# Optimization experiments

Hardware: AMD Instinct MI355X
Metric: run time of the kernel (lower is better)

The kernel has to match this reference:

```python
import math
import jax, jax.numpy as jnp
import numpy as np

B, N, D = 4, 4096, 1024
H = 16
DK = D // H  # 64
M = 256      # nb_features
EPS = 1e-6


def _gorf(key, n_rows, n_cols):
    """Gaussian orthogonal random matrix (n_rows, n_cols), stacked orthonormal
    blocks with chi-distributed row lengths (Performer GORF)."""
    blocks, rows_left = [], n_rows
    while rows_left > 0:
        br = min(n_cols, rows_left)
        key, k1, k2 = jax.random.split(key, 3)
        u = jax.random.normal(k1, (n_cols, n_cols), dtype=jnp.float32)
        q, r = jnp.linalg.qr(u)
        q = q * jnp.sign(jnp.diagonal(r))[None, :]  # q @ diag(sign(diag(r)))
        g = jax.random.normal(k2, (br, n_cols), dtype=jnp.float32)
        lengths = jnp.linalg.norm(g, axis=1, keepdims=True)
        blocks.append(q[:br] * lengths)
        rows_left -= br
    return jnp.concatenate(blocks, axis=0)


def setup_inputs() -> dict:
    key = jax.random.key(0)
    ks = jax.random.split(key, 8)
    x = jax.random.normal(ks[0], (B, N, D), dtype=jnp.float32)
    # True = PAD
    key_padding_mask = jax.random.randint(ks[1], (B, N), 0, 2).astype(jnp.bool_)
    # Linear params (xavier-scale init; exact scheme irrelevant to the math)
    Wqkv = jax.random.normal(ks[2], (3 * D, D), dtype=jnp.float32) * 0.02
    bqkv = jnp.zeros((3 * D,), dtype=jnp.float32)
    Wout = jax.random.normal(ks[3], (D, D), dtype=jnp.float32) * 0.02
    bout = jnp.zeros((D,), dtype=jnp.float32)
    # Per-head GORF omega, scaled by sqrt(dk) as in _draw_features
    omega = jnp.stack(
        [_gorf(jax.random.fold_in(ks[4], h), M, DK) for h in range(H)], axis=0
    ) * math.sqrt(DK)  # (H, M, dk)
    return {"x": x, "key_padding_mask": key_padding_mask, "Wqkv": Wqkv,
            "bqkv": bqkv, "Wout": Wout, "bout": bout, "omega": omega}


def _phi_exp(t, omega):
    # t: (B,H,N,dk) -> (B,H,N,M)
    proj = jnp.einsum('bhnd,hmd->bhnm', t, omega)
    sq_norm = 0.5 * jnp.sum(t * t, axis=-1, keepdims=True)
    z = proj - sq_norm
    z = z - jnp.max(z, axis=-1, keepdims=True)          # stabilize
    return jnp.exp(z) / math.sqrt(M + 1e-6)


def reference(x, key_padding_mask, Wqkv, bqkv, Wout, bout, omega):
    qkv = x @ Wqkv.T + bqkv                              # (B,N,3D)
    Q, K, V = jnp.split(qkv, 3, axis=-1)
    split = lambda t: t.reshape(B, N, H, DK).transpose(0, 2, 1, 3)  # (B,H,N,dk)
    Q, K, V = split(Q), split(K), split(V)
    valid_bool = ~key_padding_mask                       # (B,N), True=real token
    valid = valid_bool[:, None, :, None].astype(x.dtype) # (B,1,N,1)
    Qp = _phi_exp(Q, omega)                              # (B,H,N,M)
    Kp = _phi_exp(K, omega) * valid                      # zero PAD keys
    KV = jnp.einsum('bhnm,bhnd->bhmd', Kp, V)            # (B,H,M,dk)
    ksum = jnp.sum(Kp, axis=2)                           # (B,H,M)
    num = jnp.einsum('bhnm,bhmd->bhnd', Qp, KV)          # (B,H,N,dk)
    den = jnp.einsum('bhnm,bhm->bhn', Qp, ksum)[..., None] + EPS
    ctx = num / den                                      # (B,H,N,dk)
    out = ctx.transpose(0, 2, 1, 3).reshape(B, N, D)     # merge heads
    out = out @ Wout.T + bout
    out = out * valid_bool[..., None].astype(out.dtype)  # PAD queries -> exact 0
    return out
```

## Files before the change

kernel.cpp:

```cpp
#include <hip/hip_runtime.h>
#include <hip/hip_bf16.h>
#include <math.h>

#define B_  4
#define N_  4096
#define D_  1024
#define H_  16
#define DK_ 64
#define M_  256
#define R_  (B_*N_)
#define EPS_ 1e-6f
#define VTROWS_ 80
#define KVROWS_ 128
#define PHK_PAD 68
#define PHQ_PAD 264

typedef __bf16 bf16;
typedef __bf16 bf16x4 __attribute__((ext_vector_type(4)));
typedef __bf16 bf16x8 __attribute__((ext_vector_type(8)));
typedef _Float16 f16;
typedef _Float16 f16x4 __attribute__((ext_vector_type(4)));
typedef _Float16 f16x8 __attribute__((ext_vector_type(8)));
typedef float  f32x4  __attribute__((ext_vector_type(4)));

#define GLD(gp, lp) __builtin_amdgcn_global_load_lds( \
    (const __attribute__((address_space(1))) void*)(gp), \
    (__attribute__((address_space(3))) void*)(lp), 16, 0, 0)

#define BAR_()   __builtin_amdgcn_s_barrier()
#define SBAR_()  __builtin_amdgcn_sched_barrier(0)
#define PRIO1_() __builtin_amdgcn_s_setprio(1)
#define PRIO0_() __builtin_amdgcn_s_setprio(0)
#define LGK0_()  do { asm volatile("s_waitcnt lgkmcnt(0)"); SBAR_(); } while (0)
#define LGK8_()  asm volatile("s_waitcnt lgkmcnt(8)")
#define VMC4_()  do { asm volatile("s_waitcnt vmcnt(4)"); SBAR_(); } while (0)

__global__ __launch_bounds__(256)
void prep_all(const float* __restrict__ x, f16* __restrict__ xh,
              const float* __restrict__ Wqkv, f16* __restrict__ Wh,
              const float* __restrict__ omega, f16* __restrict__ omhi,
              f16* __restrict__ omlo,
              const float* __restrict__ Wout, bf16* __restrict__ Wob,
              float* __restrict__ KVt32, bf16* __restrict__ VT)
{
    const int bid = blockIdx.x, tid = threadIdx.x;
    if (bid < 16384) {
        int i = bid*256 + tid;
        float4 v = ((const float4*)x)[i];
        f16x4 h = { (f16)v.x, (f16)v.y, (f16)v.z, (f16)v.w };
        ((f16x4*)xh)[i] = h;
    } else if (bid < 19456) {
        int i = (bid - 16384)*256 + tid;
        float4 v = ((const float4*)Wqkv)[i];
        f16x4 h = { (f16)v.x, (f16)v.y, (f16)v.z, (f16)v.w };
        ((f16x4*)Wh)[i] = h;
    } else if (bid < 19712) {
        int i = (bid - 19456)*256 + tid;
        float4 v = ((const float4*)omega)[i];
        f16x4 h = { (f16)v.x, (f16)v.y, (f16)v.z, (f16)v.w };
        ((f16x4*)omhi)[i] = h;
        f16x4 l = { (f16)(v.x - (float)h[0]), (f16)(v.y - (float)h[1]),
                    (f16)(v.z - (float)h[2]), (f16)(v.w - (float)h[3]) };
        ((f16x4*)omlo)[i] = l;
    } else if (bid < 20736) {
        int i = (bid - 19712)*256 + tid;
        float4 v = ((const float4*)Wout)[i];
        bf16x4 h = { (bf16)v.x, (bf16)v.y, (bf16)v.z, (bf16)v.w };
        ((bf16x4*)Wob)[i] = h;
    } else if (bid < 22016) {
        int i = (bid - 20736)*256 + tid;
        ((float4*)KVt32)[i] = make_float4(0.f, 0.f, 0.f, 0.f);
    } else {
        int i = (bid - 22016)*256 + tid;
        int bh  = i >> 13;
        int rem = i & 8191;
        int row = 64 + (rem >> 9);
        int n8  = rem & 511;
        bf16 val = (row == 64) ? (bf16)1.0f : (bf16)0.0f;
        bf16x8 pk = { val, val, val, val, val, val, val, val };
        *(bf16x8*)&VT[((size_t)bh*VTROWS_ + row)*N_ + n8*8] = pk;
    }
}

__global__ __launch_bounds__(256)
void pack_kv(const float* __restrict__ KVt32, bf16* __restrict__ KVb)
{
    int i = blockIdx.x * 256 + threadIdx.x;
    if (i >= B_*H_*KVROWS_*M_) return;
    int bh  = i >> 15;
    int rem = i & 32767;
    int row = rem >> 8;
    int m   = rem & (M_-1);
    bf16 o = (bf16)0.0f;
    if (row < 64) {
        o = (bf16)KVt32[((size_t)bh*VTROWS_ + row)*M_ + m];
    } else if (row == 64) {
        o = (bf16)KVt32[((size_t)bh*VTROWS_ + 64)*M_ + m];
    } else if (row == 65) {
        float v = KVt32[((size_t)bh*VTROWS_ + 64)*M_ + m];
        o = (bf16)(v - (float)(bf16)v);
    }
    KVb[i] = o;
}

#define STAGE_(dstbuf, srcp, kt, half) do { \
    _Pragma("unroll") \
    for (int q_ = 0; q_ < 2; ++q_) { \
        int idx_ = q_*512 + tid; \
        int row_ = idx_ >> 3; \
        int seg_ = (idx_ & 7) ^ (row_ & 7); \
        GLD((srcp) + (size_t)((half)*128 + row_) * D_ + (kt)*64 + seg_*8, \
            &(dstbuf)[(half)*8192 + idx_*8]); \
    } } while (0)

#define LDA_G(T, buf, i0) do { \
    _Pragma("unroll") \
    for (int i_ = 0; i_ < 4; ++i_) { \
        _Pragma("unroll") \
        for (int k_ = 0; k_ < 2; ++k_) { \
            int row_ = warp_m*128 + ((i0)+i_)*16 + m16; \
            int off_ = (row_*128 + k_*64 + quad*16) ^ ((row_ & 7) << 4); \
            a[i_][k_] = *(const T*)((const char*)(buf) + off_); \
        } } } while (0)

#define LDB_G(T, buf, j0) do { \
    _Pragma("unroll") \
    for (int j_ = 0; j_ < 2; ++j_) { \
        _Pragma("unroll") \
        for (int k_ = 0; k_ < 2; ++k_) { \
            int row_ = warp_n*64 + ((j0)+j_)*16 + m16; \
            int off_ = (row_*128 + k_*64 + quad*16) ^ ((row_ & 7) << 4); \
            b[(j0)+j_][k_] = *(const T*)((const char*)(buf) + off_); \
        } } } while (0)

#define MFMA_F16N(I0, J0) do { \
    _Pragma("unroll") \
    for (int i_ = 0; i_ < 4; ++i_) \
        _Pragma("unroll") \
        for (int j_ = 0; j_ < 2; ++j_) \
            _Pragma("unroll") \
            for (int k_ = 0; k_ < 2; ++k_) \
                acc[(I0)+i_][(J0)+j_] = __builtin_amdgcn_mfma_f32_16x16x32_f16( \
                    a[i_][k_], b[(J0)+j_][k_], acc[(I0)+i_][(J0)+j_], 0, 0, 0); \
    } while (0)

#define MFMA_F16S(I0, J0) do { \
    _Pragma("unroll") \
    for (int i_ = 0; i_ < 4; ++i_) \
        _Pragma("unroll") \
        for (int j_ = 0; j_ < 2; ++j_) \
            _Pragma("unroll") \
            for (int k_ = 0; k_ < 2; ++k_) \
                acc[(I0)+i_][(J0)+j_] = __builtin_amdgcn_mfma_f32_16x16x32_f16( \
                    b[(J0)+j_][k_], a[i_][k_], acc[(I0)+i_][(J0)+j_], 0, 0, 0); \
    } while (0)

#define MFMA_BF16S(I0, J0) do { \
    _Pragma("unroll") \
    for (int i_ = 0; i_ < 4; ++i_) \
        _Pragma("unroll") \
        for (int j_ = 0; j_ < 2; ++j_) \
            _Pragma("unroll") \
            for (int k_ = 0; k_ < 2; ++k_) \
                acc[(I0)+i_][(J0)+j_] = __builtin_amdgcn_mfma_f32_16x16x32_bf16( \
                    b[(J0)+j_][k_], a[i_][k_], acc[(I0)+i_][(J0)+j_], 0, 0, 0); \
    } while (0)

#define KLOOP_8PH(MFMA_OP) \
    STAGE_(sA[0], gA, 0, 0); \
    STAGE_(sA[0], gA, 0, 1); \
    STAGE_(sB[0], gB, 0, 0); \
    STAGE_(sB[0], gB, 0, 1); \
    STAGE_(sB[1], gB, 1, 0); \
    STAGE_(sB[1], gB, 1, 1); \
    VMC4_(); \
    BAR_(); \
    for (int it = 0; it < 8; ++it) { \
        const int t1 = 2*it + 1, t2 = 2*it + 2, t3 = 2*it + 3; \
        LDA_G(FRAG_T, sA[0], 0); LDB_G(FRAG_T, sB[0], 0); \
        STAGE_(sA[1], gA, t1, 0); \
        LGK8_(); \
        BAR_(); LGK0_(); \
        PRIO1_(); MFMA_OP(0, 0); PRIO0_(); \
        BAR_(); \
        LDB_G(FRAG_T, sB[0], 2); \
        STAGE_(sA[1], gA, t1, 1); \
        BAR_(); LGK0_(); \
        PRIO1_(); MFMA_OP(0, 2); PRIO0_(); \
        BAR_(); \
        LDA_G(FRAG_T, sA[0], 4); \
        if (t2 < 16) STAGE_(sB[0], gB, t2, 0); \
        BAR_(); LGK0_(); \
        PRIO1_(); MFMA_OP(4, 2); PRIO0_(); \
        BAR_(); \
        if (t2 < 16) STAGE_(sB[0], gB, t2, 1); \
        VMC4_(); \
        BAR_(); \
        PRIO1_(); MFMA_OP(4, 0); PRIO0_(); \
        BAR_(); \
        LDA_G(FRAG_T, sA[1], 0); LDB_G(FRAG_T, sB[1], 0); \
        if (t2 < 16) STAGE_(sA[0], gA, t2, 0); \
        LGK8_(); \
        BAR_(); LGK0_(); \
        PRIO1_(); MFMA_OP(0, 0); PRIO0_(); \
        BAR_(); \
        LDB_G(FRAG_T, sB[1], 2); \
        if (t2 < 16) STAGE_(sA[0], gA, t2, 1); \
        BAR_(); LGK0_(); \
        PRIO1_(); MFMA_OP(0, 2); PRIO0_(); \
        BAR_(); \
        LDA_G(FRAG_T, sA[1], 4); \
        if (t3 < 16) STAGE_(sB[1], gB, t3, 0); \
        BAR_(); LGK0_(); \
        PRIO1_(); MFMA_OP(4, 2); PRIO0_(); \
        BAR_(); \
        if (t3 < 16) STAGE_(sB[1], gB, t3, 1); \
        VMC4_(); \
        BAR_(); \
        PRIO1_(); MFMA_OP(4, 0); PRIO0_(); \
        BAR_(); \
    }

#define FRAG_T f16x8
__global__ __launch_bounds__(512)
void gemm_qkv_all(const f16* __restrict__ X, const f16* __restrict__ Wh,
                  const float* __restrict__ bqkv,
                  f16* __restrict__ Qh, f16* __restrict__ Kh,
                  bf16* __restrict__ VT)
{
    __shared__ __align__(16) f16 sA[2][256*64];
    __shared__ __align__(16) f16 sB[2][256*64];
    const int tid = threadIdx.x;

    const int nwg = gridDim.x * gridDim.y;
    int flat = blockIdx.y * gridDim.x + blockIdx.x;
    int wgid = (flat & 7) * (nwg >> 3) + (flat >> 3);
    const int bm  = (wgid / 12) * 256;
    const int bnx = wgid % 12;

    const int lane = tid & 63, wave = tid >> 6;
    const int warp_m = wave >> 2, warp_n = wave & 3;
    const int m16 = lane & 15, quad = lane >> 4;

    f32x4 acc[8][4];
    #pragma unroll
    for (int i = 0; i < 8; ++i)
        #pragma unroll
        for (int j = 0; j < 4; ++j)
            acc[i][j] = (f32x4){0.f, 0.f, 0.f, 0.f};
    f16x8 a[4][2], b[4][2];

    if (bnx < 8) {
        const int bn = bnx * 256;
        const f16* gA = X  + (size_t)bm * D_;
        const f16* gB = Wh + (size_t)bn * D_;

        KLOOP_8PH(MFMA_F16S)

        f16* outp = (bn >= D_) ? Kh : Qh;
        const int cofs = (bn >= D_) ? D_ : 0;
        #pragma unroll
        for (int j = 0; j < 4; ++j) {
            int gcol0 = bn + warp_n*64 + j*16 + quad*4;
            float4 bv = *(const float4*)&bqkv[gcol0];
            int col0 = gcol0 - cofs;
            #pragma unroll
            for (int i = 0; i < 8; ++i) {
                int row = bm + warp_m*128 + i*16 + m16;
                f16x4 pk = { (f16)(acc[i][j][0] + bv.x), (f16)(acc[i][j][1] + bv.y),
                             (f16)(acc[i][j][2] + bv.z), (f16)(acc[i][j][3] + bv.w) };
                *(f16x4*)&outp[(size_t)row * D_ + col0] = pk;
            }
        }
    } else {
        const int bn = 2*D_ + (bnx - 8) * 256;
        const f16* gA = X  + (size_t)bm * D_;
        const f16* gB = Wh + (size_t)bn * D_;

        KLOOP_8PH(MFMA_F16N)

        #pragma unroll
        for (int j = 0; j < 4; ++j) {
            int gcol = bn + warp_n*64 + j*16 + m16;
            float bv = bqkv[gcol];
            int vcol = gcol - 2*D_;
            int hh = vcol >> 6, dd = vcol & 63;
            #pragma unroll
            for (int i = 0; i < 8; ++i) {
                int row0 = bm + warp_m*128 + i*16 + quad*4;
                int bb = row0 >> 12, nn = row0 & (N_-1);
                bf16x4 pk = { (bf16)(acc[i][j][0]+bv), (bf16)(acc[i][j][1]+bv),
                              (bf16)(acc[i][j][2]+bv), (bf16)(acc[i][j][3]+bv) };
                *(bf16x4*)&VT[(((size_t)bb*H_+hh)*VTROWS_ + dd)*N_ + nn] = pk;
            }
        }
    }
}
#undef FRAG_T

#define FRAG_T bf16x8
__global__ __launch_bounds__(512)
void gemm_out8(const bf16* __restrict__ A, const bf16* __restrict__ W,
               const float* __restrict__ bias, float* __restrict__ C,
               const int* __restrict__ mask)
{
    __shared__ __align__(16) bf16 sA[2][256*64];
    __shared__ __align__(16) bf16 sB[2][256*64];
    const int tid = threadIdx.x;

    const int nwg = gridDim.x * gridDim.y;
    int flat = blockIdx.y * gridDim.x + blockIdx.x;
    int wgid = (flat & 7) * (nwg >> 3) + (flat >> 3);
    const int bm = (wgid >> 2) * 256;
    const int bn = (wgid & 3) * 256;

    const int lane = tid & 63, wave = tid >> 6;
    const int warp_m = wave >> 2, warp_n = wave & 3;
    const int m16 = lane & 15, quad = lane >> 4;

    const bf16* gA = A + (size_t)bm * D_;
    const bf16* gB = W + (size_t)bn * D_;

    f32x4 acc[8][4];
    #pragma unroll
    for (int i = 0; i < 8; ++i)
        #pragma unroll
        for (int j = 0; j < 4; ++j)
            acc[i][j] = (f32x4){0.f, 0.f, 0.f, 0.f};
    bf16x8 a[4][2], b[4][2];

    KLOOP_8PH(MFMA_BF16S)

    #pragma unroll
    for (int j = 0; j < 4; ++j) {
        int col0 = bn + warp_n*64 + j*16 + quad*4;
        float4 bv = *(const float4*)&bias[col0];
        #pragma unroll
        for (int i = 0; i < 8; ++i) {
            int row = bm + warp_m*128 + i*16 + m16;
            float4 v;
            if (mask[row] != 0) {
                v = make_float4(0.f, 0.f, 0.f, 0.f);
            } else {
                v = make_float4(acc[i][j][0] + bv.x, acc[i][j][1] + bv.y,
                                acc[i][j][2] + bv.z, acc[i][j][3] + bv.w);
            }
            *(float4*)&C[(size_t)row * D_ + col0] = v;
        }
    }
}
#undef FRAG_T

#define STAGEK_(sub_, bi_) do { \
    const int n0_ = nsp*1024 + (sub_)*128; \
    _Pragma("unroll") \
    for (int it_ = 0; it_ < 2; ++it_) { \
        int idx_ = it_*512 + tid; \
        int row_ = idx_ >> 3, seg_ = (idx_ & 7) ^ (row_ & 7); \
        GLD(Kh + (size_t)(b*N_ + n0_ + row_) * D_ + h*DK_ + seg_*8, \
            &sK[bi_][idx_*8]); \
    } } while (0)

#define STAGEVT_(sub_) do { \
    const int n0_ = nsp*1024 + (sub_)*128; \
    _Pragma("unroll") \
    for (int it_ = 0; it_ < 2; ++it_) { \
        int idx_ = it_*512 + tid; \
        int row_ = idx_ >> 4, seg_ = (idx_ & 15) ^ (row_ & 7); \
        GLD(VT + ((size_t)bh*VTROWS_ + row_)*N_ + n0_ + seg_*8, \
            &sVT[idx_*8]); \
    } \
    if (tid < 256) { \
        int idx_ = 1024 + tid; \
        int row_ = idx_ >> 4, seg_ = (idx_ & 15) ^ (row_ & 7); \
        GLD(VT + ((size_t)bh*VTROWS_ + row_)*N_ + n0_ + seg_*8, \
            &sVT[idx_*8]); \
    } } while (0)

#define STAGEOM_(arr_, src_) do { \
    _Pragma("unroll") \
    for (int q_ = 0; q_ < 4; ++q_) { \
        int idx_ = q_*512 + tid; \
        int row_ = idx_ >> 3, seg_ = (idx_ & 7) ^ (row_ & 7); \
        GLD((src_) + (size_t)row_*DK_ + seg_*8, &(arr_)[idx_*8]); \
    } } while (0)

__global__ __launch_bounds__(512, 1)
void fused_kv(const f16* __restrict__ Kh, const bf16* __restrict__ VT,
              const f16* __restrict__ omhi, const f16* __restrict__ omlo,
              const int* __restrict__ mask, float* __restrict__ KVt32)
{
    __shared__ __align__(16) f16  sK[2][128*64];
    __shared__ __align__(16) bf16 sVT[VTROWS_*128];
    __shared__ __align__(16) f16  sOmH[M_*DK_];
    __shared__ __align__(16) f16  sOmL[M_*DK_];
    __shared__ __align__(16) bf16 sPhi[M_*PHK_PAD];
    const int nsp = blockIdx.x;
    const int h = blockIdx.y, b = blockIdx.z;
    const int bh = b*H_ + h;
    const int tid = threadIdx.x, lane = tid & 63, wave = tid >> 6;
    const int m16 = lane & 15, quad = lane >> 4;
    const int wm = wave * 32;
    const int nloc = wave*16 + quad*4;
    const float inv_sqrt_m = rsqrtf((float)M_ + 1e-6f);
    const f16* omh = omhi + (size_t)h * M_ * DK_;
    const f16* oml = omlo + (size_t)h * M_ * DK_;

    f32x4 kvacc[5][2];
    #pragma unroll
    for (int d = 0; d < 5; ++d)
        #pragma unroll
        for (int j = 0; j < 2; ++j)
            kvacc[d][j] = (f32x4){0.f, 0.f, 0.f, 0.f};

    STAGEOM_(sOmH, omh);
    STAGEOM_(sOmL, oml);
    STAGEK_(0, 0);

    for (int sub = 0; sub < 8; ++sub) {
        const int cur = sub & 1;
        const int n0 = nsp*1024 + sub*128;

        asm volatile("s_waitcnt vmcnt(0) lgkmcnt(0)");
        SBAR_();
        BAR_();

        int4 mv4 = *(const int4*)&mask[b*N_ + n0 + nloc];
        const int* mv = (const int*)&mv4;
        STAGEVT_(sub);
        if (sub < 7) STAGEK_(sub+1, cur^1);

        const char* kb = (const char*)&sK[cur][0];
        const int rowb = wave*16 + m16;
        f16x8 ah0 = *(const f16x8*)(kb + ((rowb*128 +      quad*16) ^ ((rowb & 7) << 4)));
        f16x8 ah1 = *(const f16x8*)(kb + ((rowb*128 + 64 + quad*16) ^ ((rowb & 7) << 4)));

        f32x4 acc[16];
        #pragma unroll
        for (int j = 0; j < 16; ++j) acc[j] = (f32x4){0.f, 0.f, 0.f, 0.f};

        PRIO1_();
        #pragma unroll
        for (int j = 0; j < 16; ++j) {
            int rowm = j*16 + m16;
            int bo0 = (rowm*128 +      quad*16) ^ ((rowm & 7) << 4);
            int bo1 = (rowm*128 + 64 + quad*16) ^ ((rowm & 7) << 4);
            f16x8 bh0 = *(const f16x8*)((const char*)sOmH + bo0);
            f16x8 bh1 = *(const f16x8*)((const char*)sOmH + bo1);
            f16x8 bl0 = *(const f16x8*)((const char*)sOmL + bo0);
            f16x8 bl1 = *(const f16x8*)((const char*)sOmL + bo1);
            acc[j] = __builtin_amdgcn_mfma_f32_16x16x32_f16(ah0, bh0, acc[j], 0,0,0);
            acc[j] = __builtin_amdgcn_mfma_f32_16x16x32_f16(ah0, bl0, acc[j], 0,0,0);
            acc[j] = __builtin_amdgcn_mfma_f32_16x16x32_f16(ah1, bh1, acc[j], 0,0,0);
            acc[j] = __builtin_amdgcn_mfma_f32_16x16x32_f16(ah1, bl1, acc[j], 0,0,0);
        }
        PRIO0_();

        #pragma unroll
        for (int r = 0; r < 4; ++r) {
            float mx = acc[0][r];
            #pragma unroll
            for (int j = 1; j < 16; ++j) mx = fmaxf(mx, acc[j][r]);
            mx = fmaxf(mx, __shfl_xor(mx, 1, 64));
            mx = fmaxf(mx, __shfl_xor(mx, 2, 64));
            mx = fmaxf(mx, __shfl_xor(mx, 4, 64));
            mx = fmaxf(mx, __shfl_xor(mx, 8, 64));
            #pragma unroll
            for (int j = 0; j < 16; ++j)
                acc[j][r] = __expf(acc[j][r] - mx) * inv_sqrt_m;
        }

        if (wave < 4) {
            #pragma unroll
            for (int j = 0; j < 16; ++j) {
                bf16x4 pk;
                #pragma unroll
                for (int r = 0; r < 4; ++r)
                    pk[r] = mv[r] ? (bf16)0.0f : (bf16)acc[j][r];
                *(bf16x4*)&sPhi[(j*16 + m16)*PHK_PAD + nloc] = pk;
            }
        }
        asm volatile("s_waitcnt lgkmcnt(0)");
        if (sub < 7) { asm volatile("s_waitcnt vmcnt(2)"); }
        else         { asm volatile("s_waitcnt vmcnt(0)"); }
        SBAR_();
        BAR_();

        PRIO1_();
        #pragma unroll
        for (int ks = 0; ks < 2; ++ks) {
            bf16x8 av[5], bp[2];
            #pragma unroll
            for (int d = 0; d < 5; ++d) {
                int rowv = d*16 + m16;
                av[d] = *(const bf16x8*)((const char*)sVT +
                        ((rowv*256 + ks*64 + quad*16) ^ ((rowv & 7) << 4)));
            }
            #pragma unroll
            for (int j = 0; j < 2; ++j)
                bp[j] = *(const bf16x8*)&sPhi[(wm + j*16 + m16)*PHK_PAD + ks*32 + quad*8];
            #pragma unroll
            for (int d = 0; d < 5; ++d)
                #pragma unroll
                for (int j = 0; j < 2; ++j)
                    kvacc[d][j] = __builtin_amdgcn_mfma_f32_16x16x32_bf16(
                        av[d], bp[j], kvacc[d][j], 0, 0, 0);
        }
        PRIO0_();
        asm volatile("s_waitcnt lgkmcnt(0)");
        SBAR_();
        BAR_();

        if (wave >= 4) {
            #pragma unroll
            for (int j = 0; j < 16; ++j) {
                bf16x4 pk;
                #pragma unroll
                for (int r = 0; r < 4; ++r)
                    pk[r] = mv[r] ? (bf16)0.0f : (bf16)acc[j][r];
                *(bf16x4*)&sPhi[(j*16 + m16)*PHK_PAD + (nloc - 64)] = pk;
            }
        }
        asm volatile("s_waitcnt lgkmcnt(0)");
        SBAR_();
        BAR_();

        PRIO1_();
        #pragma unroll
        for (int ks = 0; ks < 2; ++ks) {
            bf16x8 av[5], bp[2];
            #pragma unroll
            for (int d = 0; d < 5; ++d) {
                int rowv = d*16 + m16;
                av[d] = *(const bf16x8*)((const char*)sVT +
                        ((rowv*256 + 128 + ks*64 + quad*16) ^ ((rowv & 7) << 4)));
            }
            #pragma unroll
            for (int j = 0; j < 2; ++j)
                bp[j] = *(const bf16x8*)&sPhi[(wm + j*16 + m16)*PHK_PAD + ks*32 + quad*8];
            #pragma unroll
            for (int d = 0; d < 5; ++d)
                #pragma unroll
                for (int j = 0; j < 2; ++j)
                    kvacc[d][j] = __builtin_amdgcn_mfma_f32_16x16x32_bf16(
                        av[d], bp[j], kvacc[d][j], 0, 0, 0);
        }
        PRIO0_();
    }

    #pragma unroll
    for (int d = 0; d < 5; ++d)
        #pragma unroll
        for (int j = 0; j < 2; ++j) {
            int drow = d*16 + quad*4;
            int m = wm + j*16 + m16;
            #pragma unroll
            for (int r = 0; r < 4; ++r)
                atomicAdd(&KVt32[((size_t)bh*VTROWS_ + drow + r)*M_ + m],
                          kvacc[d][j][r]);
        }
}

__global__ __launch_bounds__(512, 1)
void fused_ctx(const f16* __restrict__ Qh, const f16* __restrict__ omhi,
               const f16* __restrict__ omlo, const bf16* __restrict__ KVb,
               bf16* __restrict__ ctx)
{
    __shared__ __align__(16) f16  sOmH[M_*DK_];
    __shared__ __align__(16) f16  sOmL[M_*DK_];
    __shared__ __align__(16) bf16 sPhi[128*PHQ_PAD];
    __shared__ float sden[2][128];
    const int nsp = blockIdx.x;
    const int h = blockIdx.y, b = blockIdx.z;
    const int bh = b*H_ + h;
    const int tid = threadIdx.x, lane = tid & 63, wave = tid >> 6;
    const int m16 = lane & 15, quad = lane >> 4;
    const float inv_sqrt_m = rsqrtf((float)M_ + 1e-6f);
    const f16* omh = omhi + (size_t)h * M_ * DK_;
    const f16* oml = omlo + (size_t)h * M_ * DK_;

    STAGEOM_(sOmH, omh);
    STAGEOM_(sOmL, oml);
    asm volatile("s_waitcnt vmcnt(0)");
    SBAR_();
    BAR_();

    const int wq = wave >> 2;
    const int wc = wave & 3;

    for (int nb = 0; nb < 8; ++nb) {
        const int q0 = nsp*1024 + nb*128;

        const int rowq = wave*16 + m16;
        f16x8 ah0 = *(const f16x8*)&Qh[(size_t)(b*N_ + q0 + rowq)*D_ + h*DK_ + quad*8];
        f16x8 ah1 = *(const f16x8*)&Qh[(size_t)(b*N_ + q0 + rowq)*D_ + h*DK_ + 32 + quad*8];

        f32x4 acc[16];
        #pragma unroll
        for (int j = 0; j < 16; ++j) acc[j] = (f32x4){0.f, 0.f, 0.f, 0.f};

        PRIO1_();
        #pragma unroll
        for (int j = 0; j < 16; ++j) {
            int rowm = j*16 + m16;
            int bo0 = (rowm*128 +      quad*16) ^ ((rowm & 7) << 4);
            int bo1 = (rowm*128 + 64 + quad*16) ^ ((rowm & 7) << 4);
            f16x8 bh0 = *(const f16x8*)((const char*)sOmH + bo0);
            f16x8 bh1 = *(const f16x8*)((const char*)sOmH + bo1);
            f16x8 bl0 = *(const f16x8*)((const char*)sOmL + bo0);
            f16x8 bl1 = *(const f16x8*)((const char*)sOmL + bo1);
            acc[j] = __builtin_amdgcn_mfma_f32_16x16x32_f16(ah0, bh0, acc[j], 0,0,0);
            acc[j] = __builtin_amdgcn_mfma_f32_16x16x32_f16(ah0, bl0, acc[j], 0,0,0);
            acc[j] = __builtin_amdgcn_mfma_f32_16x16x32_f16(ah1, bh1, acc[j], 0,0,0);
            acc[j] = __builtin_amdgcn_mfma_f32_16x16x32_f16(ah1, bl1, acc[j], 0,0,0);
        }
        PRIO0_();

        bf16x8 wf[2][8];
        #pragma unroll
        for (int jr = 0; jr < 2; ++jr) {
            int rowk = wc*32 + jr*16 + m16;
            #pragma unroll
            for (int ks = 0; ks < 8; ++ks)
                wf[jr][ks] = *(const bf16x8*)&KVb[((size_t)bh*KVROWS_ + rowk)*M_
                                                  + ks*32 + quad*8];
        }

        #pragma unroll
        for (int r = 0; r < 4; ++r) {
            float mx = acc[0][r];
            #pragma unroll
            for (int j = 1; j < 16; ++j) mx = fmaxf(mx, acc[j][r]);
            mx = fmaxf(mx, __shfl_xor(mx, 1, 64));
            mx = fmaxf(mx, __shfl_xor(mx, 2, 64));
            mx = fmaxf(mx, __shfl_xor(mx, 4, 64));
            mx = fmaxf(mx, __shfl_xor(mx, 8, 64));
            #pragma unroll
            for (int j = 0; j < 16; ++j)
                acc[j][r] = __expf(acc[j][r] - mx) * inv_sqrt_m;
        }

        {
            int nloc0 = wave*16 + quad*4;
            #pragma unroll
            for (int j = 0; j < 16; ++j)
                #pragma unroll
                for (int r = 0; r < 4; ++r)
                    sPhi[(nloc0 + r)*PHQ_PAD + j*16 + m16] = (bf16)acc[j][r];
        }
        asm volatile("s_waitcnt lgkmcnt(0)");
        SBAR_();
        BAR_();

        f32x4 cacc[4][2];
        #pragma unroll
        for (int i = 0; i < 4; ++i)
            #pragma unroll
            for (int j = 0; j < 2; ++j)
                cacc[i][j] = (f32x4){0.f, 0.f, 0.f, 0.f};

        PRIO1_();
        #pragma unroll
        for (int ks = 0; ks < 8; ++ks) {
            bf16x8 af[4];
            #pragma unroll
            for (int i = 0; i < 4; ++i)
                af[i] = *(const bf16x8*)&sPhi[(wq*64 + i*16 + m16)*PHQ_PAD
                                              + ks*32 + quad*8];
            #pragma unroll
            for (int i = 0; i < 4; ++i)
                #pragma unroll
                for (int jr = 0; jr < 2; ++jr)
                    cacc[i][jr] = __builtin_amdgcn_mfma_f32_16x16x32_bf16(
                        af[i], wf[jr][ks], cacc[i][jr], 0, 0, 0);
        }
        PRIO0_();

        if (wc == 2 && m16 < 2) {
            #pragma unroll
            for (int i = 0; i < 4; ++i)
                #pragma unroll
                for (int r = 0; r < 4; ++r)
                    sden[m16][wq*64 + i*16 + quad*4 + r] = cacc[i][0][r];
        }
        asm volatile("s_waitcnt lgkmcnt(0)");
        SBAR_();
        BAR_();

        if (wc < 2) {
            #pragma unroll
            for (int i = 0; i < 4; ++i) {
                #pragma unroll
                for (int r = 0; r < 4; ++r) {
                    int lrow = wq*64 + i*16 + quad*4 + r;
                    float den = sden[0][lrow] + sden[1][lrow] + EPS_;
                    #pragma unroll
                    for (int jr = 0; jr < 2; ++jr)
                        ctx[(size_t)(b*N_ + q0 + lrow)*D_ + h*DK_
                            + wc*32 + jr*16 + m16] = (bf16)(cacc[i][jr][r] / den);
                }
            }
        }
        asm volatile("s_waitcnt lgkmcnt(0)");
        SBAR_();
        BAR_();
    }
}

extern "C" void kernel_launch(void* const* d_in, const int* in_sizes, int n_in,
                              void* d_out, int out_size, void* d_ws, size_t ws_size,
                              hipStream_t stream)
{
    const float* x     = (const float*)d_in[0];
    const int*   mask  = (const int*)d_in[1];
    const float* Wqkv  = (const float*)d_in[2];
    const float* bqkv  = (const float*)d_in[3];
    const float* Wout  = (const float*)d_in[4];
    const float* bout  = (const float*)d_in[5];
    const float* omega = (const float*)d_in[6];
    float* out = (float*)d_out;

    char* w = (char*)d_ws;
    f16*   Wh    = (f16*)w;    w += (size_t)3*D_*D_ * 2;
    bf16*  Wob   = (bf16*)w;   w += (size_t)D_*D_ * 2;
    f16*   omhi  = (f16*)w;    w += (size_t)H_*M_*DK_ * 2;
    f16*   omlo  = (f16*)w;    w += (size_t)H_*M_*DK_ * 2;
    f16*   xh    = (f16*)w;    w += (size_t)R_ * D_ * 2;
    f16*   Qh    = (f16*)w;    w += (size_t)R_ * D_ * 2;
    f16*   Kh    = (f16*)w;    w += (size_t)R_ * D_ * 2;
    bf16*  VT    = (bf16*)w;   w += (size_t)B_*H_*VTROWS_*N_ * 2;
    float* KVt32 = (float*)w;  w += (size_t)B_*H_*VTROWS_*M_ * 4;
    bf16*  KVb   = (bf16*)w;   w += (size_t)B_*H_*KVROWS_*M_ * 2;
    bf16*  VC    = (bf16*)Kh;

    prep_all<<<24064, 256, 0, stream>>>(x, xh, Wqkv, Wh, omega, omhi, omlo,
                                        Wout, Wob, KVt32, VT);

    gemm_qkv_all<<<dim3(12, R_/256), 512, 0, stream>>>(xh, Wh, bqkv, Qh, Kh, VT);

    fused_kv<<<dim3(4, H_, B_), 512, 0, stream>>>(Kh, VT, omhi, omlo, mask, KVt32);

    pack_kv<<<(B_*H_*KVROWS_*M_ + 255)/256, 256, 0, stream>>>(KVt32, KVb);

    fused_ctx<<<dim3(4, H_, B_), 512, 0, stream>>>(Qh, omhi, omlo, KVb, VC);

    gemm_out8<<<dim3(4, R_/256), 512, 0, stream>>>(VC, Wob, bout, out, mask);
}
```

Baseline: 423.2 us.

## Transpose Q-feature MFMA, hoist KV fragment loads, prefetch next Q tile

Swaps the MFMA operand order so each lane holds one query row's feature values, which reduces the row max to two cross-lane shuffles and lets the phi tile be written to shared memory as packed 4-wide bf16 stores. The KV fragment loads move out of the block loop since they are loop-invariant. The next block's Q fragments are now prefetched during softmax. Register pressure rises because the wf fragments and the prefetched Q stay live across the whole loop.

```diff
diff --git a/kernel.cpp b/kernel.cpp
--- a/kernel.cpp
+++ b/kernel.cpp
@@ -581,19 +581,31 @@
 
     STAGEOM_(sOmH, omh);
     STAGEOM_(sOmL, oml);
+
+    const int wq = wave >> 2;
+    const int wc = wave & 3;
+
+    bf16x8 wf[2][8];
+    #pragma unroll
+    for (int jr = 0; jr < 2; ++jr) {
+        int rowk = wc*32 + jr*16 + m16;
+        #pragma unroll
+        for (int ks = 0; ks < 8; ++ks)
+            wf[jr][ks] = *(const bf16x8*)&KVb[((size_t)bh*KVROWS_ + rowk)*M_
+                                              + ks*32 + quad*8];
+    }
+
+    const int rowq = wave*16 + m16;
+    const f16* qbase = Qh + (size_t)(b*N_ + nsp*1024 + rowq)*D_ + h*DK_;
+    f16x8 qa0 = *(const f16x8*)(qbase + quad*8);
+    f16x8 qa1 = *(const f16x8*)(qbase + 32 + quad*8);
+
     asm volatile("s_waitcnt vmcnt(0)");
     SBAR_();
     BAR_();
 
-    const int wq = wave >> 2;
-    const int wc = wave & 3;
-
     for (int nb = 0; nb < 8; ++nb) {
         const int q0 = nsp*1024 + nb*128;
-
-        const int rowq = wave*16 + m16;
-        f16x8 ah0 = *(const f16x8*)&Qh[(size_t)(b*N_ + q0 + rowq)*D_ + h*DK_ + quad*8];
-        f16x8 ah1 = *(const f16x8*)&Qh[(size_t)(b*N_ + q0 + rowq)*D_ + h*DK_ + 32 + quad*8];
 
         f32x4 acc[16];
         #pragma unroll
@@ -609,44 +621,44 @@
             f16x8 bh1 = *(const f16x8*)((const char*)sOmH + bo1);
             f16x8 bl0 = *(const f16x8*)((const char*)sOmL + bo0);
             f16x8 bl1 = *(const f16x8*)((const char*)sOmL + bo1);
-            acc[j] = __builtin_amdgcn_mfma_f32_16x16x32_f16(ah0, bh0, acc[j], 0,0,0);
-            acc[j] = __builtin_amdgcn_mfma_f32_16x16x32_f16(ah0, bl0, acc[j], 0,0,0);
-            acc[j] = __builtin_amdgcn_mfma_f32_16x16x32_f16(ah1, bh1, acc[j], 0,0,0);
-            acc[j] = __builtin_amdgcn_mfma_f32_16x16x32_f16(ah1, bl1, acc[j], 0,0,0);
+            acc[j] = __builtin_amdgcn_mfma_f32_16x16x32_f16(bh0, qa0, acc[j], 0,0,0);
+            acc[j] = __builtin_amdgcn_mfma_f32_16x16x32_f16(bl0, qa0, acc[j], 0,0,0);
+            acc[j] = __builtin_amdgcn_mfma_f32_16x16x32_f16(bh1, qa1, acc[j], 0,0,0);
+            acc[j] = __builtin_amdgcn_mfma_f32_16x16x32_f16(bl1, qa1, acc[j], 0,0,0);
         }
         PRIO0_();
 
-        bf16x8 wf[2][8];
-        #pragma unroll
-        for (int jr = 0; jr < 2; ++jr) {
-            int rowk = wc*32 + jr*16 + m16;
-            #pragma unroll
-            for (int ks = 0; ks < 8; ++ks)
-                wf[jr][ks] = *(const bf16x8*)&KVb[((size_t)bh*KVROWS_ + rowk)*M_
-                                                  + ks*32 + quad*8];
-        }
-
-        #pragma unroll
-        for (int r = 0; r < 4; ++r) {
-            float mx = acc[0][r];
-            #pragma unroll
-            for (int j = 1; j < 16; ++j) mx = fmaxf(mx, acc[j][r]);
-            mx = fmaxf(mx, __shfl_xor(mx, 1, 64));
-            mx = fmaxf(mx, __shfl_xor(mx, 2, 64));
-            mx = fmaxf(mx, __shfl_xor(mx, 4, 64));
-            mx = fmaxf(mx, __shfl_xor(mx, 8, 64));
+        f16x8 qn0, qn1;
+        if (nb < 7) {
+            const f16* qb2 = qbase + (size_t)(nb+1)*128*D_;
+            qn0 = *(const f16x8*)(qb2 + quad*8);
+            qn1 = *(const f16x8*)(qb2 + 32 + quad*8);
+        }
+
+        {
+            float mx = acc[0][0];
             #pragma unroll
             for (int j = 0; j < 16; ++j)
-                acc[j][r] = __expf(acc[j][r] - mx) * inv_sqrt_m;
+                #pragma unroll
+                for (int r = 0; r < 4; ++r)
+                    mx = fmaxf(mx, acc[j][r]);
+            mx = fmaxf(mx, __shfl_xor(mx, 16, 64));
+            mx = fmaxf(mx, __shfl_xor(mx, 32, 64));
+            #pragma unroll
+            for (int j = 0; j < 16; ++j)
+                #pragma unroll
+                for (int r = 0; r < 4; ++r)
+                    acc[j][r] = __expf(acc[j][r] - mx) * inv_sqrt_m;
         }
 
         {
-            int nloc0 = wave*16 + quad*4;
-            #pragma unroll
-            for (int j = 0; j < 16; ++j)
-                #pragma unroll
-                for (int r = 0; r < 4; ++r)
-                    sPhi[(nloc0 + r)*PHQ_PAD + j*16 + m16] = (bf16)acc[j][r];
+            const int nrow = wave*16 + m16;
+            #pragma unroll
+            for (int j = 0; j < 16; ++j) {
+                bf16x4 pk = { (bf16)acc[j][0], (bf16)acc[j][1],
+                              (bf16)acc[j][2], (bf16)acc[j][3] };
+                *(bf16x4*)&sPhi[nrow*PHQ_PAD + j*16 + quad*4] = pk;
+            }
         }
         asm volatile("s_waitcnt lgkmcnt(0)");
         SBAR_();
@@ -704,6 +716,8 @@
         asm volatile("s_waitcnt lgkmcnt(0)");
         SBAR_();
         BAR_();
+
+        if (nb < 7) { qa0 = qn0; qa1 = qn1; }
     }
 }
 
```

Measured after the change: 427.1 us. About the same (+0.9%).
